# Kernel tuning notes

Measured on AMD Instinct MI355X. Metric: run time of the kernel, lower is better.

The kernel has to match this reference:

```python
import jax, jax.numpy as jnp
import numpy as np

N_NODES = 100000
N_EDGES = 1600000
D_IN = 128
LAYER_SIZES = [128, 128, 64]


def setup_inputs() -> dict:
    key = jax.random.key(0)
    ks = jax.random.split(key, 12)
    x = jax.random.normal(ks[0], (N_NODES, D_IN), dtype=jnp.float32)
    edge_index = jax.random.randint(ks[1], (2, N_EDGES), 0, N_NODES, dtype=jnp.int64)
    edge_weight = jax.random.uniform(ks[2], (N_EDGES,), dtype=jnp.float32)
    inp = {"x": x, "edge_index": edge_index, "edge_weight": edge_weight}
    dims = [D_IN] + LAYER_SIZES
    for i in range(len(LAYER_SIZES)):
        fan_in, fan_out = dims[i], dims[i + 1]
        # glorot-style init like PyG GCNConv
        scale = jnp.sqrt(6.0 / (fan_in + fan_out)).astype(jnp.float32)
        inp[f"W{i}"] = jax.random.uniform(ks[3 + 2 * i], (fan_in, fan_out), dtype=jnp.float32, minval=-scale, maxval=scale)
        inp[f"b{i}"] = jnp.zeros((fan_out,), dtype=jnp.float32)
    return inp


def _gcn_norm(edge_index, edge_weight, num_nodes):
    # PyG gcn_norm with add_self_loops=True (fill value 1.0)
    src, dst = edge_index[0], edge_index[1]
    loop = jnp.arange(num_nodes, dtype=edge_index.dtype)
    src_full = jnp.concatenate([src, loop])
    dst_full = jnp.concatenate([dst, loop])
    w_full = jnp.concatenate([edge_weight, jnp.ones((num_nodes,), dtype=edge_weight.dtype)])
    deg = jax.ops.segment_sum(w_full, dst_full, num_segments=num_nodes)  # [N]
    deg_inv_sqrt = jnp.where(deg > 0, jax.lax.rsqrt(jnp.where(deg > 0, deg, 1.0)), 0.0)
    norm = deg_inv_sqrt[src_full] * w_full * deg_inv_sqrt[dst_full]  # [E+N]
    return src_full, dst_full, norm


def _gcn_conv(x, src, dst, norm, W, b):
    h = x @ W                                  # [N, d_out] dense transform
    msg = h[src] * norm[:, None]               # [E+N, d_out] gather + scale
    out = jax.ops.segment_sum(msg, dst, num_segments=x.shape[0])  # scatter-add
    return out + b


def reference(x, edge_index, edge_weight, W0, b0, W1, b1, W2, b2):
    N = x.shape[0]
    src, dst, norm = _gcn_norm(edge_index, edge_weight, N)
    x = jax.nn.relu(_gcn_conv(x, src, dst, norm, W0, b0))
    x = jax.nn.relu(_gcn_conv(x, src, dst, norm, W1, b1))
    x = _gcn_conv(x, src, dst, norm, W2, b2)  # no ReLU on final layer
    return x
```

## Files before the change

### kernel.cpp

```cpp
#include <hip/hip_runtime.h>
#include <hip/hip_fp16.h>


typedef __attribute__((ext_vector_type(8))) _Float16 f16x8;
typedef __attribute__((ext_vector_type(4))) float f32x4;
typedef unsigned long long u64;

#define WQ_BITS 15
#define WQ_SCALE 32768.0f
#define WQ_MASK 32767u
#define MAXNP 2048

#define SHFLU(v, k) ((unsigned int)__shfl((int)(v), (k), 64))

__global__ __launch_bounds__(256) void k_pre(int* tail, int NP,
                                             const float* __restrict__ W0,
                                             const float* __restrict__ W1,
                                             const float* __restrict__ W2,
                                             __half* __restrict__ wt0,
                                             __half* __restrict__ wt1,
                                             __half* __restrict__ wt2) {
    int id = blockIdx.x * 256 + threadIdx.x;
    if (id < NP) tail[id] = 0;
    if (id < 16384) {
        int n = id >> 7, k = id & 127;
        wt0[id] = __float2half(W0[k * 128 + n]);
    } else if (id < 32768) {
        int j = id - 16384, n = j >> 7, k = j & 127;
        wt1[j] = __float2half(W1[k * 128 + n]);
    } else if (id < 40960) {
        int j = id - 32768, n = j >> 7, k = j & 127;
        wt2[j] = __float2half(W2[k * 64 + n]);
    }
}

__global__ __launch_bounds__(256) void k_bin(const int* __restrict__ src,
                                             const int* __restrict__ dst,
                                             const float* __restrict__ w,
                                             int* tail, u64* __restrict__ glist,
                                             int E, int ecap, int NP, int shift) {
    __shared__ unsigned int h[MAXNP];
    __shared__ int base[MAXNP];
    const int nb = gridDim.x;
    const int per = (E + nb - 1) / nb;
    const int e0 = blockIdx.x * per;
    const int e1 = (e0 + per < E) ? e0 + per : E;

    for (int i = threadIdx.x; i < NP; i += 256) h[i] = 0;
    __syncthreads();
    for (int e = e0 + (int)threadIdx.x; e < e1; e += 256) {
        int p = dst[e] >> shift;
        atomicAdd(&h[p], 1u);
    }
    __syncthreads();
    for (int i = threadIdx.x; i < NP; i += 256) {
        unsigned int c = h[i];
        base[i] = c ? atomicAdd(&tail[i], (int)c) : 0;
    }
    __syncthreads();
    for (int e = e0 + (int)threadIdx.x; e < e1; e += 256) {
        int t = dst[e];
        int p = t >> shift;
        int s = __builtin_nontemporal_load(src + e);
        float we = __builtin_nontemporal_load(w + e);
        int wq = (int)(we * WQ_SCALE + 0.5f);
        wq = (wq < (int)WQ_MASK) ? wq : (int)WQ_MASK;
        u64 v = ((u64)(unsigned)t << 32) |
                ((unsigned)s << WQ_BITS) | (unsigned)wq;
        unsigned int idx = atomicSub(&h[p], 1u) - 1u;
        int pos = base[p] + (int)idx;
        if (pos < ecap) glist[(size_t)p * ecap + pos] = v;
    }
}

__global__ __launch_bounds__(256) void k_fill(const int* __restrict__ tail,
                                              const u64* __restrict__ glist,
                                              int ecap, int* __restrict__ cnt,
                                              float* __restrict__ dinv,
                                              unsigned int* __restrict__ EW,
                                              int cap, int N, int shift) {
    __shared__ unsigned int lcnt[MAXNP];
    __shared__ float lws[MAXNP];
    const int p = blockIdx.x;
    const int np = 1 << shift;
    const int t0 = p << shift;
    for (int i = threadIdx.x; i < np; i += 256) { lcnt[i] = 0; lws[i] = 0.f; }
    __syncthreads();
    int n = tail[p];
    if (n > ecap) n = ecap;
    const u64* L = glist + (size_t)p * ecap;
    for (int j = threadIdx.x; j < n; j += 256) {
        u64 v = L[j];
        int t = (int)(v >> 32);
        int loc = t - t0;
        unsigned int k = atomicAdd(&lcnt[loc], 1u);
        if ((int)k < cap) {
            EW[(size_t)t * cap + k] = (unsigned int)v;
            atomicAdd(&lws[loc], (float)((unsigned int)v & WQ_MASK));
        }
    }
    __syncthreads();
    for (int i = threadIdx.x; i < np; i += 256) {
        int t = t0 + i;
        if (t < N) {
            int c = (int)lcnt[i];
            c = (c < cap) ? c : cap;
            cnt[t] = c;
            dinv[t] = 1.0f / sqrtf(1.0f + lws[i] * (1.0f / WQ_SCALE));
        }
    }
}

template <int BN, bool XFP32>
__global__ __launch_bounds__(256, 4) void k_gemm(const void* __restrict__ Xv,
                                                 const __half* __restrict__ Wt,
                                                 const float* __restrict__ dinv,
                                                 __half* __restrict__ H, int N) {
    const int tid = threadIdx.x;
    const int lane = tid & 63;
    const int wv = tid >> 6;
    const int m = lane & 15;
    const int quad = lane >> 4;
    const int rb = blockIdx.x * 64;
    const int row = rb + wv * 16 + m;
    const int rowc = (row < N) ? row : (N - 1);

    f16x8 xf[4];
    if constexpr (XFP32) {
        const float* X = (const float*)Xv;
#pragma unroll
        for (int s = 0; s < 4; s++) {
            const float4* p = (const float4*)(X + (size_t)rowc * 128 + s * 32 + quad * 8);
            float4 u0 = p[0], u1 = p[1];
            f16x8 f;
            f[0] = (_Float16)u0.x; f[1] = (_Float16)u0.y;
            f[2] = (_Float16)u0.z; f[3] = (_Float16)u0.w;
            f[4] = (_Float16)u1.x; f[5] = (_Float16)u1.y;
            f[6] = (_Float16)u1.z; f[7] = (_Float16)u1.w;
            xf[s] = f;
        }
    } else {
        const __half* X = (const __half*)Xv;
#pragma unroll
        for (int s = 0; s < 4; s++)
            xf[s] = *(const f16x8*)(X + (size_t)rowc * 128 + s * 32 + quad * 8);
    }

    constexpr int NT = BN / 16;
    f32x4 acc[NT];
#pragma unroll
    for (int t = 0; t < NT; t++) acc[t] = (f32x4){0.f, 0.f, 0.f, 0.f};

#pragma unroll
    for (int s = 0; s < 4; s++) {
#pragma unroll
        for (int t = 0; t < NT; t++) {
            f16x8 wf = *(const f16x8*)(Wt + (size_t)(t * 16 + m) * 128 + s * 32 + quad * 8);
            acc[t] = __builtin_amdgcn_mfma_f32_16x16x32_f16(wf, xf[s], acc[t], 0, 0, 0);
        }
    }

    if (row < N) {
        float sc = dinv[row];
#pragma unroll
        for (int t = 0; t < NT; t++) {
            __half2 h0 = __floats2half2_rn(sc * acc[t][0], sc * acc[t][1]);
            __half2 h1 = __floats2half2_rn(sc * acc[t][2], sc * acc[t][3]);
            __half2* dstp = (__half2*)(H + (size_t)row * BN + t * 16 + quad * 4);
            dstp[0] = h0;
            dstp[1] = h1;
        }
    }
}

template <int DOUT, bool RELU>
__global__ __launch_bounds__(256) void k_agg(const __half* __restrict__ H,
                                             const unsigned int* __restrict__ EW,
                                             const int* __restrict__ cnt,
                                             const float* __restrict__ dinv,
                                             const float* __restrict__ bias,
                                             void* __restrict__ Outv,
                                             int N, int cap) {
    int node = blockIdx.x * 4 + (threadIdx.x >> 6);
    if (node >= N) return;
    const int lane = threadIdx.x & 63;

    int c = cnt[node];
    c = (c < cap) ? c : cap;

    unsigned int meta = 0;
    if (lane < c) meta = EW[(size_t)node * cap + lane];

    float dt = dinv[node];

    if constexpr (DOUT == 128) {
        const int part = lane & 15;
        const int q = lane >> 4;
        float acc[8];
#pragma unroll
        for (int j = 0; j < 8; j++) acc[j] = 0.f;

        int k = 0;
        for (; k + 16 <= c; k += 16) {
            f16x8 hv[4];
            float w[4];
#pragma unroll
            for (int g = 0; g < 4; g++) {
                unsigned int mm = SHFLU(meta, k + g * 4 + q);
                w[g] = (float)(mm & WQ_MASK) * (1.0f / WQ_SCALE);
                hv[g] = *(const f16x8*)(H + (size_t)(mm >> WQ_BITS) * 128 + part * 8);
            }
#pragma unroll
            for (int g = 0; g < 4; g++)
#pragma unroll
                for (int j = 0; j < 8; j++)
                    acc[j] = fmaf(w[g], (float)hv[g][j], acc[j]);
        }
        for (; k < c; k += 4) {
            int idx = k + q;
            unsigned int mm = SHFLU(meta, (idx < c) ? idx : 0);
            float w = (idx < c) ? (float)(mm & WQ_MASK) * (1.0f / WQ_SCALE) : 0.f;
            unsigned int row = (idx < c) ? (mm >> WQ_BITS) : (unsigned int)node;
            f16x8 hv = *(const f16x8*)(H + (size_t)row * 128 + part * 8);
#pragma unroll
            for (int j = 0; j < 8; j++)
                acc[j] = fmaf(w, (float)hv[j], acc[j]);
        }
#pragma unroll
        for (int j = 0; j < 8; j++) {
            acc[j] += __shfl_xor(acc[j], 16, 64);
            acc[j] += __shfl_xor(acc[j], 32, 64);
        }
        if (q == 0) {
            f16x8 sv = *(const f16x8*)(H + (size_t)node * 128 + part * 8);
            f32x4 b0v = *(const f32x4*)(bias + part * 8);
            f32x4 b1v = *(const f32x4*)(bias + part * 8 + 4);
            f16x8 ov;
#pragma unroll
            for (int j = 0; j < 8; j++) {
                float bj = (j < 4) ? b0v[j] : b1v[j - 4];
                float v = fmaf(dt, acc[j] + (float)sv[j], bj);
                if (RELU) v = fmaxf(v, 0.f);
                ov[j] = (_Float16)v;
            }
            *(f16x8*)((__half*)Outv + (size_t)node * 128 + part * 8) = ov;
        }
    } else {
        const int part = lane & 7;
        const int q = lane >> 3;
        float acc[8];
#pragma unroll
        for (int j = 0; j < 8; j++) acc[j] = 0.f;

        int k = 0;
        for (; k + 32 <= c; k += 32) {
            f16x8 hv[4];
            float w[4];
#pragma unroll
            for (int g = 0; g < 4; g++) {
                unsigned int mm = SHFLU(meta, k + g * 8 + q);
                w[g] = (float)(mm & WQ_MASK) * (1.0f / WQ_SCALE);
                hv[g] = *(const f16x8*)(H + (size_t)(mm >> WQ_BITS) * 64 + part * 8);
            }
#pragma unroll
            for (int g = 0; g < 4; g++)
#pragma unroll
                for (int j = 0; j < 8; j++)
                    acc[j] = fmaf(w[g], (float)hv[g][j], acc[j]);
        }
        for (; k < c; k += 8) {
            int idx = k + q;
            unsigned int mm = SHFLU(meta, (idx < c) ? idx : 0);
            float w = (idx < c) ? (float)(mm & WQ_MASK) * (1.0f / WQ_SCALE) : 0.f;
            unsigned int row = (idx < c) ? (mm >> WQ_BITS) : (unsigned int)node;
            f16x8 hv = *(const f16x8*)(H + (size_t)row * 64 + part * 8);
#pragma unroll
            for (int j = 0; j < 8; j++)
                acc[j] = fmaf(w, (float)hv[j], acc[j]);
        }
#pragma unroll
        for (int j = 0; j < 8; j++) {
            acc[j] += __shfl_xor(acc[j], 8, 64);
            acc[j] += __shfl_xor(acc[j], 16, 64);
            acc[j] += __shfl_xor(acc[j], 32, 64);
        }
        if (q == 0) {
            f16x8 sv = *(const f16x8*)(H + (size_t)node * 64 + part * 8);
            f32x4 b0v = *(const f32x4*)(bias + part * 8);
            f32x4 b1v = *(const f32x4*)(bias + part * 8 + 4);
            f32x4 o0, o1;
#pragma unroll
            for (int j = 0; j < 8; j++) {
                float bj = (j < 4) ? b0v[j] : b1v[j - 4];
                float v = fmaf(dt, acc[j] + (float)sv[j], bj);
                if (RELU) v = fmaxf(v, 0.f);
                if (j < 4) o0[j] = v; else o1[j - 4] = v;
            }
            float* op = (float*)Outv + (size_t)node * 64 + part * 8;
            *(f32x4*)op = o0;
            *(f32x4*)(op + 4) = o1;
        }
    }
}

extern "C" void kernel_launch(void* const* d_in, const int* in_sizes, int n_in,
                              void* d_out, int out_size, void* d_ws, size_t ws_size,
                              hipStream_t stream) {
    const int N = in_sizes[0] / 128;
    const int E = in_sizes[2];

    const float* x  = (const float*)d_in[0];
    const int*   ei = (const int*)d_in[1];
    const int*   src = ei;
    const int*   dst = ei + E;
    const float* ew  = (const float*)d_in[2];
    const float* W0 = (const float*)d_in[3];
    const float* b0 = (const float*)d_in[4];
    const float* W1 = (const float*)d_in[5];
    const float* b1 = (const float*)d_in[6];
    const float* W2 = (const float*)d_in[7];
    const float* b2 = (const float*)d_in[8];

    int shift = 6;
    while ((((N - 1) >> shift) + 1) > MAXNP) shift++;
    const int NP = ((N - 1) >> shift) + 1;

    size_t fixed = (((size_t)N * 4 + 255) & ~(size_t)255)
                 + (((size_t)N * 4 + 255) & ~(size_t)255)
                 + 2 * (((size_t)N * 128 * 2 + 255) & ~(size_t)255)
                 + 3 * 33024
                 + (((size_t)NP * 4 + 255) & ~(size_t)255)
                 + 2048;
    int cap = 64;
    if (ws_size > fixed) {
        size_t avail = (ws_size - fixed) / ((size_t)N * 4);
        if (avail < (size_t)cap) cap = (int)avail;
    } else {
        cap = 0;
    }

    char* p = (char*)d_ws;
    auto alloc = [&](size_t bytes) -> void* {
        void* r = (void*)p;
        p += (bytes + 255) & ~(size_t)255;
        return r;
    };
    int*          cnt  = (int*)alloc((size_t)N * 4);
    float*        dinv = (float*)alloc((size_t)N * 4);
    unsigned int* EW   = (unsigned int*)alloc((size_t)N * cap * 4);
    __half*       bufH = (__half*)alloc((size_t)N * 128 * 2);
    __half*       bufA = (__half*)alloc((size_t)N * 128 * 2);
    __half*       wt0  = (__half*)alloc(16384 * 2);
    __half*       wt1  = (__half*)alloc(16384 * 2);
    __half*       wt2  = (__half*)alloc(8192 * 2);
    int*          tail = (int*)alloc((size_t)NP * 4);

    u64* glist = (u64*)bufH;
    int  ecap  = (int)(((size_t)N * 128 * 2) / ((size_t)NP * 8));

    dim3 blk(256);
    int preN = (NP > 40960) ? NP : 40960;
    dim3 gPre((preN + 255) / 256);
    dim3 gBin(256);
    dim3 gFill(NP);
    dim3 gGemm((N + 63) / 64);
    dim3 gWave((N + 3) / 4);

    k_pre<<<gPre, blk, 0, stream>>>(tail, NP, W0, W1, W2, wt0, wt1, wt2);
    k_bin<<<gBin, blk, 0, stream>>>(src, dst, ew, tail, glist, E, ecap, NP, shift);
    k_fill<<<gFill, blk, 0, stream>>>(tail, glist, ecap, cnt, dinv, EW, cap, N, shift);

    k_gemm<128, true><<<gGemm, blk, 0, stream>>>(x, wt0, dinv, bufH, N);
    k_agg<128, true><<<gWave, blk, 0, stream>>>(bufH, EW, cnt, dinv, b0, bufA, N, cap);

    k_gemm<128, false><<<gGemm, blk, 0, stream>>>(bufA, wt1, dinv, bufH, N);
    k_agg<128, true><<<gWave, blk, 0, stream>>>(bufH, EW, cnt, dinv, b1, bufA, N, cap);

    k_gemm<64, false><<<gGemm, blk, 0, stream>>>(bufA, wt2, dinv, bufH, N);
    k_agg<64, false><<<gWave, blk, 0, stream>>>(bufH, EW, cnt, dinv, b2,
                                                d_out, N, cap);
}
```

Measured before the change: 427.3 us.

## Fuse CSR fill kernel with first-layer GEMM per node partition

Merges the per-partition edge fill kernel with the first-layer dense transform. Each fill block now computes dinv into shared memory and then runs the MFMA GEMM for its own node range, scaling rows directly from shared memory. This removes one kernel launch and a dinv round trip. The edge list scratch moves to bufA so the GEMM can write into bufH. The cost is that the GEMM now runs on only NP blocks, each looping over its partition, so parallelism and occupancy may be lower than the separate GEMM grid had.

```diff
diff --git a/kernel.cpp b/kernel.cpp
--- a/kernel.cpp
+++ b/kernel.cpp
@@ -73,17 +73,18 @@
     }
 }
 
-__global__ __launch_bounds__(256) void k_fill(const int* __restrict__ tail,
-                                              const u64* __restrict__ glist,
-                                              int ecap, int* __restrict__ cnt,
-                                              float* __restrict__ dinv,
-                                              unsigned int* __restrict__ EW,
-                                              int cap, int N, int shift) {
+__global__ __launch_bounds__(256) void k_fillgemm0(
+    const int* __restrict__ tail, const u64* __restrict__ glist, int ecap,
+    int* __restrict__ cnt, float* __restrict__ dinv,
+    unsigned int* __restrict__ EW, int cap, int N, int shift,
+    const float* __restrict__ X, const __half* __restrict__ Wt,
+    __half* __restrict__ H) {
     __shared__ unsigned int lcnt[MAXNP];
     __shared__ float lws[MAXNP];
     const int p = blockIdx.x;
     const int np = 1 << shift;
     const int t0 = p << shift;
+
     for (int i = threadIdx.x; i < np; i += 256) { lcnt[i] = 0; lws[i] = 0.f; }
     __syncthreads();
     int n = tail[p];
@@ -102,17 +103,68 @@
     __syncthreads();
     for (int i = threadIdx.x; i < np; i += 256) {
         int t = t0 + i;
+        float dv = 1.0f / sqrtf(1.0f + lws[i] * (1.0f / WQ_SCALE));
         if (t < N) {
             int c = (int)lcnt[i];
             c = (c < cap) ? c : cap;
             cnt[t] = c;
-            dinv[t] = 1.0f / sqrtf(1.0f + lws[i] * (1.0f / WQ_SCALE));
-        }
-    }
-}
-
-template <int BN, bool XFP32>
-__global__ __launch_bounds__(256, 4) void k_gemm(const void* __restrict__ Xv,
+            dinv[t] = dv;
+        }
+        lws[i] = dv;
+    }
+    __syncthreads();
+
+    const int lane = threadIdx.x & 63;
+    const int wv = threadIdx.x >> 6;
+    const int m = lane & 15;
+    const int quad = lane >> 4;
+    for (int rb = 0; rb < np; rb += 64) {
+        const int rloc = rb + wv * 16 + m;
+        const int row = t0 + rloc;
+        const int rowc = (row < N) ? row : (N - 1);
+
+        f16x8 xf[4];
+#pragma unroll
+        for (int s = 0; s < 4; s++) {
+            const float4* pp = (const float4*)(X + (size_t)rowc * 128 + s * 32 + quad * 8);
+            float4 u0 = pp[0], u1 = pp[1];
+            f16x8 f;
+            f[0] = (_Float16)u0.x; f[1] = (_Float16)u0.y;
+            f[2] = (_Float16)u0.z; f[3] = (_Float16)u0.w;
+            f[4] = (_Float16)u1.x; f[5] = (_Float16)u1.y;
+            f[6] = (_Float16)u1.z; f[7] = (_Float16)u1.w;
+            xf[s] = f;
+        }
+
+        f32x4 acc[8];
+#pragma unroll
+        for (int t = 0; t < 8; t++) acc[t] = (f32x4){0.f, 0.f, 0.f, 0.f};
+
+#pragma unroll
+        for (int s = 0; s < 4; s++) {
+#pragma unroll
+            for (int t = 0; t < 8; t++) {
+                f16x8 wf = *(const f16x8*)(Wt + (size_t)(t * 16 + m) * 128 + s * 32 + quad * 8);
+                acc[t] = __builtin_amdgcn_mfma_f32_16x16x32_f16(wf, xf[s], acc[t], 0, 0, 0);
+            }
+        }
+
+        if (row < N) {
+            float sc = lws[rloc];
+#pragma unroll
+            for (int t = 0; t < 8; t++) {
+                __half2 h0 = __floats2half2_rn(sc * acc[t][0], sc * acc[t][1]);
+                __half2 h1 = __floats2half2_rn(sc * acc[t][2], sc * acc[t][3]);
+                __half2* dstp = (__half2*)(H + (size_t)row * 128 + t * 16 + quad * 4);
+                dstp[0] = h0;
+                dstp[1] = h1;
+            }
+        }
+    }
+}
+
+template <int BN>
+__global__ __launch_bounds__(256, 4) void k_gemm(const __half* __restrict__ X,
                                                  const __half* __restrict__ Wt,
                                                  const float* __restrict__ dinv,
                                                  __half* __restrict__ H, int N) {
@@ -126,25 +178,9 @@
     const int rowc = (row < N) ? row : (N - 1);
 
     f16x8 xf[4];
-    if constexpr (XFP32) {
-        const float* X = (const float*)Xv;
-#pragma unroll
-        for (int s = 0; s < 4; s++) {
-            const float4* p = (const float4*)(X + (size_t)rowc * 128 + s * 32 + quad * 8);
-            float4 u0 = p[0], u1 = p[1];
-            f16x8 f;
-            f[0] = (_Float16)u0.x; f[1] = (_Float16)u0.y;
-            f[2] = (_Float16)u0.z; f[3] = (_Float16)u0.w;
-            f[4] = (_Float16)u1.x; f[5] = (_Float16)u1.y;
-            f[6] = (_Float16)u1.z; f[7] = (_Float16)u1.w;
-            xf[s] = f;
-        }
-    } else {
-        const __half* X = (const __half*)Xv;
-#pragma unroll
-        for (int s = 0; s < 4; s++)
-            xf[s] = *(const f16x8*)(X + (size_t)rowc * 128 + s * 32 + quad * 8);
-    }
+#pragma unroll
+    for (int s = 0; s < 4; s++)
+        xf[s] = *(const f16x8*)(X + (size_t)rowc * 128 + s * 32 + quad * 8);
 
     constexpr int NT = BN / 16;
     f32x4 acc[NT];
@@ -355,7 +391,7 @@
     __half*       wt2  = (__half*)alloc(8192 * 2);
     int*          tail = (int*)alloc((size_t)NP * 4);
 
-    u64* glist = (u64*)bufH;
+    u64* glist = (u64*)bufA;
     int  ecap  = (int)(((size_t)N * 128 * 2) / ((size_t)NP * 8));
 
     dim3 blk(256);
@@ -368,15 +404,15 @@
 
     k_pre<<<gPre, blk, 0, stream>>>(tail, NP, W0, W1, W2, wt0, wt1, wt2);
     k_bin<<<gBin, blk, 0, stream>>>(src, dst, ew, tail, glist, E, ecap, NP, shift);
-    k_fill<<<gFill, blk, 0, stream>>>(tail, glist, ecap, cnt, dinv, EW, cap, N, shift);
-
-    k_gemm<128, true><<<gGemm, blk, 0, stream>>>(x, wt0, dinv, bufH, N);
+
+    k_fillgemm0<<<gFill, blk, 0, stream>>>(tail, glist, ecap, cnt, dinv, EW,
+                                           cap, N, shift, x, wt0, bufH);
     k_agg<128, true><<<gWave, blk, 0, stream>>>(bufH, EW, cnt, dinv, b0, bufA, N, cap);
 
-    k_gemm<128, false><<<gGemm, blk, 0, stream>>>(bufA, wt1, dinv, bufH, N);
+    k_gemm<128><<<gGemm, blk, 0, stream>>>(bufA, wt1, dinv, bufH, N);
     k_agg<128, true><<<gWave, blk, 0, stream>>>(bufH, EW, cnt, dinv, b1, bufA, N, cap);
 
-    k_gemm<64, false><<<gGemm, blk, 0, stream>>>(bufA, wt2, dinv, bufH, N);
+    k_gemm<64><<<gGemm, blk, 0, stream>>>(bufA, wt2, dinv, bufH, N);
     k_agg<64, false><<<gWave, blk, 0, stream>>>(bufH, EW, cnt, dinv, b2,
                                                 d_out, N, cap);
 }
```

Result: no change. 425.9 us (-0.3%).

## Reorder GCN layers to aggregate-then-transform and fuse aggregation with GEMM

Applied to the files above, without the earlier changes.

Each layer now aggregates the dinv-prescaled input features over neighbors (Â·X), then multiplies by W inside the same kernel using an LDS tile and MFMA, instead of running GEMM then a separate gather/scatter kernel. The first layer's input is prescaled and converted to fp16 in k_fill, which removes the separate GEMM launches and their intermediate round-trip through HBM. The cost is that the last layer now gathers 128-wide rows instead of 64-wide, and each block covers only 16 nodes, so a wave handles 4 nodes serially.

```diff
diff --git a/kernel.cpp b/kernel.cpp
--- a/kernel.cpp
+++ b/kernel.cpp
@@ -10,6 +10,7 @@
 #define WQ_SCALE 32768.0f
 #define WQ_MASK 32767u
 #define MAXNP 2048
+#define TSTR 136
 
 #define SHFLU(v, k) ((unsigned int)__shfl((int)(v), (k), 64))
 
@@ -78,12 +79,15 @@
                                               int ecap, int* __restrict__ cnt,
                                               float* __restrict__ dinv,
                                               unsigned int* __restrict__ EW,
-                                              int cap, int N, int shift) {
+                                              int cap, int N, int shift,
+                                              const float* __restrict__ X,
+                                              __half* __restrict__ As0) {
     __shared__ unsigned int lcnt[MAXNP];
     __shared__ float lws[MAXNP];
     const int p = blockIdx.x;
     const int np = 1 << shift;
     const int t0 = p << shift;
+
     for (int i = threadIdx.x; i < np; i += 256) { lcnt[i] = 0; lws[i] = 0.f; }
     __syncthreads();
     int n = tail[p];
@@ -102,51 +106,124 @@
     __syncthreads();
     for (int i = threadIdx.x; i < np; i += 256) {
         int t = t0 + i;
+        float dv = 1.0f / sqrtf(1.0f + lws[i] * (1.0f / WQ_SCALE));
         if (t < N) {
             int c = (int)lcnt[i];
             c = (c < cap) ? c : cap;
             cnt[t] = c;
-            dinv[t] = 1.0f / sqrtf(1.0f + lws[i] * (1.0f / WQ_SCALE));
-        }
-    }
-}
-
-template <int BN, bool XFP32>
-__global__ __launch_bounds__(256, 4) void k_gemm(const void* __restrict__ Xv,
-                                                 const __half* __restrict__ Wt,
-                                                 const float* __restrict__ dinv,
-                                                 __half* __restrict__ H, int N) {
+            dinv[t] = dv;
+        }
+        lws[i] = dv;
+    }
+    __syncthreads();
+
+    for (int rb = 0; rb < np; rb += 64) {
+        int rloc = rb + (int)(threadIdx.x >> 2);
+        int sub = threadIdx.x & 3;
+        int r = t0 + rloc;
+        if (rloc < np && r < N) {
+            float dv = lws[rloc];
+#pragma unroll
+            for (int cc = 0; cc < 4; cc++) {
+                int c0 = sub * 32 + cc * 8;
+                float4 u0 = *(const float4*)(X + (size_t)r * 128 + c0);
+                float4 u1 = *(const float4*)(X + (size_t)r * 128 + c0 + 4);
+                f16x8 f;
+                f[0] = (_Float16)(dv * u0.x); f[1] = (_Float16)(dv * u0.y);
+                f[2] = (_Float16)(dv * u0.z); f[3] = (_Float16)(dv * u0.w);
+                f[4] = (_Float16)(dv * u1.x); f[5] = (_Float16)(dv * u1.y);
+                f[6] = (_Float16)(dv * u1.z); f[7] = (_Float16)(dv * u1.w);
+                *(f16x8*)(As0 + (size_t)r * 128 + c0) = f;
+            }
+        }
+    }
+}
+
+template <int BNO, bool RELU, bool FINAL>
+__global__ __launch_bounds__(256) void k_layer(const __half* __restrict__ As,
+                                               const unsigned int* __restrict__ EW,
+                                               const int* __restrict__ cnt,
+                                               const float* __restrict__ dinv,
+                                               const __half* __restrict__ Wt,
+                                               const float* __restrict__ bias,
+                                               void* __restrict__ Outv,
+                                               int N, int cap) {
+    __shared__ __align__(16) __half T[16][TSTR];
     const int tid = threadIdx.x;
     const int lane = tid & 63;
     const int wv = tid >> 6;
+    const int base = blockIdx.x * 16;
+
+    for (int i = tid; i < 16 * TSTR; i += 256) ((__half*)T)[i] = (__half)0.f;
+    __syncthreads();
+
+    const int part = lane & 15;
+    const int q = lane >> 4;
+    for (int i = 0; i < 4; i++) {
+        const int rloc = wv * 4 + i;
+        const int node = base + rloc;
+        if (node < N) {
+            int c = cnt[node];
+            c = (c < cap) ? c : cap;
+            unsigned int meta = 0;
+            if (lane < c) meta = EW[(size_t)node * cap + lane];
+
+            float acc[8];
+#pragma unroll
+            for (int j = 0; j < 8; j++) acc[j] = 0.f;
+
+            int k = 0;
+            for (; k + 16 <= c; k += 16) {
+                f16x8 hv[4];
+                float w[4];
+#pragma unroll
+                for (int g = 0; g < 4; g++) {
+                    unsigned int mm = SHFLU(meta, k + g * 4 + q);
+                    w[g] = (float)(mm & WQ_MASK) * (1.0f / WQ_SCALE);
+                    hv[g] = *(const f16x8*)(As + (size_t)(mm >> WQ_BITS) * 128 + part * 8);
+                }
+#pragma unroll
+                for (int g = 0; g < 4; g++)
+#pragma unroll
+                    for (int j = 0; j < 8; j++)
+                        acc[j] = fmaf(w[g], (float)hv[g][j], acc[j]);
+            }
+            for (; k < c; k += 4) {
+                int idx = k + q;
+                unsigned int mm = SHFLU(meta, (idx < c) ? idx : 0);
+                float w = (idx < c) ? (float)(mm & WQ_MASK) * (1.0f / WQ_SCALE) : 0.f;
+                unsigned int row = (idx < c) ? (mm >> WQ_BITS) : (unsigned int)node;
+                f16x8 hv = *(const f16x8*)(As + (size_t)row * 128 + part * 8);
+#pragma unroll
+                for (int j = 0; j < 8; j++)
+                    acc[j] = fmaf(w, (float)hv[j], acc[j]);
+            }
+#pragma unroll
+            for (int j = 0; j < 8; j++) {
+                acc[j] += __shfl_xor(acc[j], 16, 64);
+                acc[j] += __shfl_xor(acc[j], 32, 64);
+            }
+            if (q == 0) {
+                f16x8 sv = *(const f16x8*)(As + (size_t)node * 128 + part * 8);
+                f16x8 tv;
+#pragma unroll
+                for (int j = 0; j < 8; j++)
+                    tv[j] = (_Float16)(acc[j] + (float)sv[j]);
+                *(f16x8*)&T[rloc][part * 8] = tv;
+            }
+        }
+    }
+    __syncthreads();
+
     const int m = lane & 15;
     const int quad = lane >> 4;
-    const int rb = blockIdx.x * 64;
-    const int row = rb + wv * 16 + m;
-    const int rowc = (row < N) ? row : (N - 1);
+    constexpr int NT = (BNO == 128) ? 2 : 1;
 
     f16x8 xf[4];
-    if constexpr (XFP32) {
-        const float* X = (const float*)Xv;
-#pragma unroll
-        for (int s = 0; s < 4; s++) {
-            const float4* p = (const float4*)(X + (size_t)rowc * 128 + s * 32 + quad * 8);
-            float4 u0 = p[0], u1 = p[1];
-            f16x8 f;
-            f[0] = (_Float16)u0.x; f[1] = (_Float16)u0.y;
-            f[2] = (_Float16)u0.z; f[3] = (_Float16)u0.w;
-            f[4] = (_Float16)u1.x; f[5] = (_Float16)u1.y;
-            f[6] = (_Float16)u1.z; f[7] = (_Float16)u1.w;
-            xf[s] = f;
-        }
-    } else {
-        const __half* X = (const __half*)Xv;
-#pragma unroll
-        for (int s = 0; s < 4; s++)
-            xf[s] = *(const f16x8*)(X + (size_t)rowc * 128 + s * 32 + quad * 8);
-    }
-
-    constexpr int NT = BN / 16;
+#pragma unroll
+    for (int s = 0; s < 4; s++)
+        xf[s] = *(const f16x8*)&T[m][s * 32 + quad * 8];
+
     f32x4 acc[NT];
 #pragma unroll
     for (int t = 0; t < NT; t++) acc[t] = (f32x4){0.f, 0.f, 0.f, 0.f};
@@ -155,150 +232,39 @@
     for (int s = 0; s < 4; s++) {
 #pragma unroll
         for (int t = 0; t < NT; t++) {
-            f16x8 wf = *(const f16x8*)(Wt + (size_t)(t * 16 + m) * 128 + s * 32 + quad * 8);
+            const int ct = wv * NT + t;
+            f16x8 wf = *(const f16x8*)(Wt + (size_t)(ct * 16 + m) * 128 + s * 32 + quad * 8);
             acc[t] = __builtin_amdgcn_mfma_f32_16x16x32_f16(wf, xf[s], acc[t], 0, 0, 0);
         }
     }
 
+    const int row = base + m;
     if (row < N) {
-        float sc = dinv[row];
+        float dt = dinv[row];
 #pragma unroll
         for (int t = 0; t < NT; t++) {
-            __half2 h0 = __floats2half2_rn(sc * acc[t][0], sc * acc[t][1]);
-            __half2 h1 = __floats2half2_rn(sc * acc[t][2], sc * acc[t][3]);
-            __half2* dstp = (__half2*)(H + (size_t)row * BN + t * 16 + quad * 4);
-            dstp[0] = h0;
-            dstp[1] = h1;
-        }
-    }
-}
-
-template <int DOUT, bool RELU>
-__global__ __launch_bounds__(256) void k_agg(const __half* __restrict__ H,
-                                             const unsigned int* __restrict__ EW,
-                                             const int* __restrict__ cnt,
-                                             const float* __restrict__ dinv,
-                                             const float* __restrict__ bias,
-                                             void* __restrict__ Outv,
-                                             int N, int cap) {
-    int node = blockIdx.x * 4 + (threadIdx.x >> 6);
-    if (node >= N) return;
-    const int lane = threadIdx.x & 63;
-
-    int c = cnt[node];
-    c = (c < cap) ? c : cap;
-
-    unsigned int meta = 0;
-    if (lane < c) meta = EW[(size_t)node * cap + lane];
-
-    float dt = dinv[node];
-
-    if constexpr (DOUT == 128) {
-        const int part = lane & 15;
-        const int q = lane >> 4;
-        float acc[8];
-#pragma unroll
-        for (int j = 0; j < 8; j++) acc[j] = 0.f;
-
-        int k = 0;
-        for (; k + 16 <= c; k += 16) {
-            f16x8 hv[4];
-            float w[4];
-#pragma unroll
-            for (int g = 0; g < 4; g++) {
-                unsigned int mm = SHFLU(meta, k + g * 4 + q);
-                w[g] = (float)(mm & WQ_MASK) * (1.0f / WQ_SCALE);
-                hv[g] = *(const f16x8*)(H + (size_t)(mm >> WQ_BITS) * 128 + part * 8);
-            }
-#pragma unroll
-            for (int g = 0; g < 4; g++)
-#pragma unroll
-                for (int j = 0; j < 8; j++)
-                    acc[j] = fmaf(w[g], (float)hv[g][j], acc[j]);
-        }
-        for (; k < c; k += 4) {
-            int idx = k + q;
-            unsigned int mm = SHFLU(meta, (idx < c) ? idx : 0);
-            float w = (idx < c) ? (float)(mm & WQ_MASK) * (1.0f / WQ_SCALE) : 0.f;
-            unsigned int row = (idx < c) ? (mm >> WQ_BITS) : (unsigned int)node;
-            f16x8 hv = *(const f16x8*)(H + (size_t)row * 128 + part * 8);
-#pragma unroll
-            for (int j = 0; j < 8; j++)
-                acc[j] = fmaf(w, (float)hv[j], acc[j]);
-        }
-#pragma unroll
-        for (int j = 0; j < 8; j++) {
-            acc[j] += __shfl_xor(acc[j], 16, 64);
-            acc[j] += __shfl_xor(acc[j], 32, 64);
-        }
-        if (q == 0) {
-            f16x8 sv = *(const f16x8*)(H + (size_t)node * 128 + part * 8);
-            f32x4 b0v = *(const f32x4*)(bias + part * 8);
-            f32x4 b1v = *(const f32x4*)(bias + part * 8 + 4);
-            f16x8 ov;
-#pragma unroll
-            for (int j = 0; j < 8; j++) {
-                float bj = (j < 4) ? b0v[j] : b1v[j - 4];
-                float v = fmaf(dt, acc[j] + (float)sv[j], bj);
-                if (RELU) v = fmaxf(v, 0.f);
-                ov[j] = (_Float16)v;
-            }
-            *(f16x8*)((__half*)Outv + (size_t)node * 128 + part * 8) = ov;
-        }
-    } else {
-        const int part = lane & 7;
-        const int q = lane >> 3;
-        float acc[8];
-#pragma unroll
-        for (int j = 0; j < 8; j++) acc[j] = 0.f;
-
-        int k = 0;
-        for (; k + 32 <= c; k += 32) {
-            f16x8 hv[4];
-            float w[4];
-#pragma unroll
-            for (int g = 0; g < 4; g++) {
-                unsigned int mm = SHFLU(meta, k + g * 8 + q);
-                w[g] = (float)(mm & WQ_MASK) * (1.0f / WQ_SCALE);
-                hv[g] = *(const f16x8*)(H + (size_t)(mm >> WQ_BITS) * 64 + part * 8);
-            }
-#pragma unroll
-            for (int g = 0; g < 4; g++)
-#pragma unroll
-                for (int j = 0; j < 8; j++)
-                    acc[j] = fmaf(w[g], (float)hv[g][j], acc[j]);
-        }
-        for (; k < c; k += 8) {
-            int idx = k + q;
-            unsigned int mm = SHFLU(meta, (idx < c) ? idx : 0);
-            float w = (idx < c) ? (float)(mm & WQ_MASK) * (1.0f / WQ_SCALE) : 0.f;
-            unsigned int row = (idx < c) ? (mm >> WQ_BITS) : (unsigned int)node;
-            f16x8 hv = *(const f16x8*)(H + (size_t)row * 64 + part * 8);
-#pragma unroll
-            for (int j = 0; j < 8; j++)
-                acc[j] = fmaf(w, (float)hv[j], acc[j]);
-        }
-#pragma unroll
-        for (int j = 0; j < 8; j++) {
-            acc[j] += __shfl_xor(acc[j], 8, 64);
-            acc[j] += __shfl_xor(acc[j], 16, 64);
-            acc[j] += __shfl_xor(acc[j], 32, 64);
-        }
-        if (q == 0) {
-            f16x8 sv = *(const f16x8*)(H + (size_t)node * 64 + part * 8);
-            f32x4 b0v = *(const f32x4*)(bias + part * 8);
-            f32x4 b1v = *(const f32x4*)(bias + part * 8 + 4);
-            f32x4 o0, o1;
-#pragma unroll
-            for (int j = 0; j < 8; j++) {
-                float bj = (j < 4) ? b0v[j] : b1v[j - 4];
-                float v = fmaf(dt, acc[j] + (float)sv[j], bj);
-                if (RELU) v = fmaxf(v, 0.f);
-                if (j < 4) o0[j] = v; else o1[j - 4] = v;
-            }
-            float* op = (float*)Outv + (size_t)node * 64 + part * 8;
-            *(f32x4*)op = o0;
-            *(f32x4*)(op + 4) = o1;
+            const int ct = wv * NT + t;
+            const int col0 = ct * 16 + quad * 4;
+            f32x4 bv = *(const f32x4*)(bias + col0);
+            float v0 = fmaf(dt, acc[t][0], bv[0]);
+            float v1 = fmaf(dt, acc[t][1], bv[1]);
+            float v2 = fmaf(dt, acc[t][2], bv[2]);
+            float v3 = fmaf(dt, acc[t][3], bv[3]);
+            if (RELU) {
+                v0 = fmaxf(v0, 0.f); v1 = fmaxf(v1, 0.f);
+                v2 = fmaxf(v2, 0.f); v3 = fmaxf(v3, 0.f);
+            }
+            if constexpr (!FINAL) {
+                __half2 h0 = __floats2half2_rn(dt * v0, dt * v1);
+                __half2 h1 = __floats2half2_rn(dt * v2, dt * v3);
+                __half2* dstp = (__half2*)((__half*)Outv + (size_t)row * 128 + col0);
+                dstp[0] = h0;
+                dstp[1] = h1;
+            } else {
+                f32x4 o;
+                o[0] = v0; o[1] = v1; o[2] = v2; o[3] = v3;
+                *(f32x4*)((float*)Outv + (size_t)row * 64 + col0) = o;
+            }
         }
     }
 }
@@ -355,7 +321,7 @@
     __half*       wt2  = (__half*)alloc(8192 * 2);
     int*          tail = (int*)alloc((size_t)NP * 4);
 
-    u64* glist = (u64*)bufH;
+    u64* glist = (u64*)bufA;
     int  ecap  = (int)(((size_t)N * 128 * 2) / ((size_t)NP * 8));
 
     dim3 blk(256);
@@ -363,20 +329,17 @@
     dim3 gPre((preN + 255) / 256);
     dim3 gBin(256);
     dim3 gFill(NP);
-    dim3 gGemm((N + 63) / 64);
-    dim3 gWave((N + 3) / 4);
+    dim3 gLayer((N + 15) / 16);
 
     k_pre<<<gPre, blk, 0, stream>>>(tail, NP, W0, W1, W2, wt0, wt1, wt2);
     k_bin<<<gBin, blk, 0, stream>>>(src, dst, ew, tail, glist, E, ecap, NP, shift);
-    k_fill<<<gFill, blk, 0, stream>>>(tail, glist, ecap, cnt, dinv, EW, cap, N, shift);
-
-    k_gemm<128, true><<<gGemm, blk, 0, stream>>>(x, wt0, dinv, bufH, N);
-    k_agg<128, true><<<gWave, blk, 0, stream>>>(bufH, EW, cnt, dinv, b0, bufA, N, cap);
-
-    k_gemm<128, false><<<gGemm, blk, 0, stream>>>(bufA, wt1, dinv, bufH, N);
-    k_agg<128, true><<<gWave, blk, 0, stream>>>(bufH, EW, cnt, dinv, b1, bufA, N, cap);
-
-    k_gemm<64, false><<<gGemm, blk, 0, stream>>>(bufA, wt2, dinv, bufH, N);
-    k_agg<64, false><<<gWave, blk, 0, stream>>>(bufH, EW, cnt, dinv, b2,
-                                                d_out, N, cap);
-}
+    k_fill<<<gFill, blk, 0, stream>>>(tail, glist, ecap, cnt, dinv, EW, cap, N,
+                                      shift, x, bufH);
+
+    k_layer<128, true, false><<<gLayer, blk, 0, stream>>>(bufH, EW, cnt, dinv,
+                                                          wt0, b0, bufA, N, cap);
+    k_layer<128, true, false><<<gLayer, blk, 0, stream>>>(bufA, EW, cnt, dinv,
+                                                          wt1, b1, bufH, N, cap);
+    k_layer<64, false, true><<<gLayer, blk, 0, stream>>>(bufH, EW, cnt, dinv,
+                                                         wt2, b2, d_out, N, cap);
+}
```

After: 410.7 us. -3.9%, faster.
